# Kernel tuning notes

Hardware: AMD Instinct MI355X
Metric: run time of the kernel (lower is better)

Reference implementation:

```python
import jax, jax.numpy as jnp
import numpy as np

# hyperparameters from init_kwargs
STEPSZ = 0.1
ALPHA = 0.01
BETA = 0.01
NSTEPS = 50
DMAX = 15.0
EXTGRADFAC = 10.0
B, H, W, N = 2, 256, 256, 128


def _bilerp(field, pts):
    # field: [H, W]; pts: [N, 2] as (row, col) float coords -> [N]
    h, w = field.shape
    y = jnp.clip(pts[:, 0], 0.0, h - 1.001)
    x = jnp.clip(pts[:, 1], 0.0, w - 1.001)
    y0 = jnp.floor(y).astype(jnp.int32)
    x0 = jnp.floor(x).astype(jnp.int32)
    y1 = y0 + 1
    x1 = x0 + 1
    wy = y - y0.astype(field.dtype)
    wx = x - x0.astype(field.dtype)
    return (field[y0, x0] * (1 - wy) * (1 - wx)
            + field[y0, x1] * (1 - wy) * wx
            + field[y1, x0] * wy * (1 - wx)
            + field[y1, x1] * wy * wx)


def _evolve(pred, nodes):
    # pred: [H, W] distance-map prediction; nodes: [N, 2] closed-contour points
    gy = jnp.gradient(pred, axis=0)
    gx = jnp.gradient(pred, axis=1)
    hi = jnp.array([pred.shape[0] - 1.0, pred.shape[1] - 1.0], dtype=pred.dtype)

    def step(x, _):
        # internal forces: 2nd derivative (elasticity) and 4th derivative (rigidity)
        d2 = jnp.roll(x, -1, 0) + jnp.roll(x, 1, 0) - 2.0 * x
        d4 = jnp.roll(d2, -1, 0) + jnp.roll(d2, 1, 0) - 2.0 * d2
        # external force: descend the predicted distance map
        ext = -EXTGRADFAC * jnp.stack([_bilerp(gy, x), _bilerp(gx, x)], axis=-1)
        x = x + STEPSZ * (ALPHA * d2 - BETA * d4 + ext)
        x = jnp.clip(x, 0.0, hi)
        return x, None

    x, _ = jax.lax.scan(step, nodes, None, length=NSTEPS)
    return x


def _render(nodes):
    # distance from every pixel to the nearest snake segment, clamped at DMAX
    yy, xx = jnp.meshgrid(jnp.arange(H, dtype=nodes.dtype),
                          jnp.arange(W, dtype=nodes.dtype), indexing='ij')
    q = jnp.stack([yy, xx], axis=-1).reshape(-1, 2)          # [P, 2]
    p0 = nodes                                               # [N, 2]
    p1 = jnp.roll(nodes, -1, 0)                              # closed contour
    d = p1 - p0                                              # [N, 2]
    dd = jnp.sum(d * d, axis=-1) + 1e-8                      # [N]
    qp = q[:, None, :] - p0[None, :, :]                      # [P, N, 2]
    t = jnp.clip(jnp.sum(qp * d[None], axis=-1) / dd, 0.0, 1.0)  # [P, N]
    r = qp - t[..., None] * d[None]                          # residual to projection
    dist = jnp.sqrt(jnp.sum(r * r, axis=-1) + 1e-12)         # [P, N]
    return jnp.minimum(dist.min(axis=1), DMAX).reshape(H, W)


def setup_inputs() -> dict:
    key = jax.random.key(0)
    k1, k2 = jax.random.split(key)
    pred_dmap = jax.random.normal(k1, (B, 1, H, W), dtype=jnp.float32)
    # snake control points spread over the image
    nodes = jax.random.uniform(k2, (B, N, 2), dtype=jnp.float32) * (H - 1.0)
    return {"pred_dmap": pred_dmap, "nodes": nodes}


def reference(pred_dmap, nodes):
    pred = pred_dmap[:, 0]                                   # [B, H, W] (detached in torch)
    final_nodes = jax.vmap(_evolve)(jax.lax.stop_gradient(pred), nodes)
    snake_dm = jax.vmap(_render)(final_nodes)[:, None]       # [B, 1, H, W]
    snake_dm = jax.lax.stop_gradient(snake_dm)               # noGrad: snake path detached
    loss = jnp.mean(jnp.square(pred_dmap - snake_dm))
    return loss
```

## Files before the change

kernel.cpp:

```cpp
#include <hip/hip_runtime.h>

#define HH 256
#define WW 256
#define NB 2
#define NN 128
#define NSTEPS_K 50
#define NBLK 256
#define MAGIC_G 0x11C0FFEE
#define MAGIC_E 0x22C0FFEE
#define MAGIC_R 0x33C0FFEE
#define SPIN_G 200000
#define SPIN_E 60000
#define SPIN_R 60000

#define WS_PART   0
#define WS_GFLG   256
#define WS_RFLG   512
#define WS_EREP   1024
#define WS_FNODE  2048
#define WS_FIELD  4096
#define WS_NEEDED_BYTES ((WS_FIELD + (size_t)NB * HH * WW * 2) * 4)

static __device__ __forceinline__ int ld_i(int* p) {
    return __hip_atomic_load(p, __ATOMIC_RELAXED, __HIP_MEMORY_SCOPE_AGENT);
}
static __device__ __forceinline__ void st_i(int* p, int v) {
    __hip_atomic_store(p, v, __ATOMIC_RELAXED, __HIP_MEMORY_SCOPE_AGENT);
}
static __device__ __forceinline__ unsigned long long ld_u64(unsigned long long* p) {
    return __hip_atomic_load(p, __ATOMIC_RELAXED, __HIP_MEMORY_SCOPE_AGENT);
}
static __device__ __forceinline__ void st_u64(unsigned long long* p, unsigned long long v) {
    __hip_atomic_store(p, v, __ATOMIC_RELAXED, __HIP_MEMORY_SCOPE_AGENT);
}
static __device__ __forceinline__ float ld_f(float* p) {
    return __hip_atomic_load(p, __ATOMIC_RELAXED, __HIP_MEMORY_SCOPE_AGENT);
}
static __device__ __forceinline__ void st_f(float* p, float v) {
    __hip_atomic_store(p, v, __ATOMIC_RELAXED, __HIP_MEMORY_SCOPE_AGENT);
}
union F2U { float2 f2; unsigned long long u; };

__global__ __launch_bounds__(1024) void fused2_kernel(
        const float* __restrict__ pred,
        const float* __restrict__ nodes_in,
        float* __restrict__ ws,
        float* __restrict__ out) {
    float* partials = ws + WS_PART;
    int*   g_flags  = (int*)(ws + WS_GFLG);
    int*   r_flags  = (int*)(ws + WS_RFLG);
    int*   e_rep    = (int*)(ws + WS_EREP);
    unsigned long long* fnodes_u = (unsigned long long*)(ws + WS_FNODE);
    unsigned long long* field_u  = (unsigned long long*)(ws + WS_FIELD);
    const float2*       field_f2 = (const float2*)(ws + WS_FIELD);

    const int blk = blockIdx.x;
    const int tid = threadIdx.x;
    const int myBatch = blk >> 7;

    if (tid < 512) {
        int idx = blk * 512 + tid;
        int b = idx >> 16, p = idx & 0xFFFF;
        int i = p >> 8, j = p & (WW - 1);
        const float* f = pred + (b << 16);
        int iu = max(i - 1, 0), id = min(i + 1, HH - 1);
        int jl = max(j - 1, 0), jr = min(j + 1, WW - 1);
        float sy = (i == 0 || i == HH - 1) ? 1.0f : 0.5f;
        float sx = (j == 0 || j == WW - 1) ? 1.0f : 0.5f;
        F2U cv;
        cv.f2 = make_float2(sy * (f[(id << 8) + j] - f[(iu << 8) + j]),
                            sx * (f[(i << 8) + jr] - f[(i << 8) + jl]));
        st_u64(&field_u[idx], cv.u);
    }
    __syncthreads();
    if (tid == 0) st_i(&g_flags[blk], MAGIC_G);

    if (blk < NB) {
        const int b = blk;
        if (tid < 64) {
            int f0 = b * 128 + tid * 2;
            for (int it = 0; it < SPIN_G; ++it) {
                bool ok = (ld_i(&g_flags[f0]) == MAGIC_G) &&
                          (ld_i(&g_flags[f0 + 1]) == MAGIC_G);
                if (__all(ok)) break;
                __builtin_amdgcn_s_sleep(2);
            }
        }
        __syncthreads();

        const float2* gb = field_f2 + (b << 16);
        float acc = 0.0f;
        #pragma unroll
        for (int k = 0; k < 8; ++k) acc += gb[((k << 10) + tid) << 3].x;
        asm volatile("" :: "v"(acc));
        __syncthreads();

        if (tid < 64) {
            const int l = tid;
            const int pl = (l + 63) & 63;
            const int nl = (l + 1) & 63;
            float4 nd = ((const float4*)nodes_in)[b * 64 + l];
            float y0n = nd.x, x0n = nd.y;
            float y1n = nd.z, x1n = nd.w;

            __builtin_amdgcn_s_setprio(1);
            for (int s = 0; s < NSTEPS_K; ++s) {
                float yca = fminf(fmaxf(y0n, 0.0f), 254.999f);
                float xca = fminf(fmaxf(x0n, 0.0f), 254.999f);
                int ra = (int)yca, ca = (int)xca;
                float wya = yca - (float)ra, wxa = xca - (float)ca;
                int basea = (ra << 8) + ca;
                float2 a00 = gb[basea],       a01 = gb[basea + 1];
                float2 a10 = gb[basea + WW],  a11 = gb[basea + WW + 1];

                float ycb = fminf(fmaxf(y1n, 0.0f), 254.999f);
                float xcb = fminf(fmaxf(x1n, 0.0f), 254.999f);
                int rb = (int)ycb, cb = (int)xcb;
                float wyb = ycb - (float)rb, wxb = xcb - (float)cb;
                int baseb = (rb << 8) + cb;
                float2 b00 = gb[baseb],       b01 = gb[baseb + 1];
                float2 b10 = gb[baseb + WW],  b11 = gb[baseb + WW + 1];

                float pya = __shfl(y0n, pl), pxa = __shfl(x0n, pl);
                float pyb = __shfl(y1n, pl), pxb = __shfl(x1n, pl);
                float nya = __shfl(y0n, nl), nxa = __shfl(x0n, nl);
                float nyb = __shfl(y1n, nl), nxb = __shfl(x1n, nl);

                float d2ya = (y1n + pyb) - 2.0f * y0n;
                float d2xa = (x1n + pxb) - 2.0f * x0n;
                float d2yb = (nya + y0n) - 2.0f * y1n;
                float d2xb = (nxa + x0n) - 2.0f * x1n;
                float d2pyb = (y0n + pya) - 2.0f * pyb;
                float d2pxb = (x0n + pxa) - 2.0f * pxb;
                float d2nya = (nyb + y1n) - 2.0f * nya;
                float d2nxa = (nxb + x1n) - 2.0f * nxa;

                float d4ya = (d2yb + d2pyb) - 2.0f * d2ya;
                float d4xa = (d2xb + d2pxb) - 2.0f * d2xa;
                float d4yb = (d2nya + d2ya) - 2.0f * d2yb;
                float d4xb = (d2nxa + d2xa) - 2.0f * d2xb;

                float ua = 1.0f - wya, va = 1.0f - wxa;
                float bya = a00.x * ua * va + a01.x * ua * wxa + a10.x * wya * va + a11.x * wya * wxa;
                float bxa = a00.y * ua * va + a01.y * ua * wxa + a10.y * wya * va + a11.y * wya * wxa;
                float ub = 1.0f - wyb, vb = 1.0f - wxb;
                float byb = b00.x * ub * vb + b01.x * ub * wxb + b10.x * wyb * vb + b11.x * wyb * wxb;
                float bxb = b00.y * ub * vb + b01.y * ub * wxb + b10.y * wyb * vb + b11.y * wyb * wxb;

                y0n = y0n + 0.1f * ((0.01f * d2ya - 0.01f * d4ya) + (-10.0f * bya));
                x0n = x0n + 0.1f * ((0.01f * d2xa - 0.01f * d4xa) + (-10.0f * bxa));
                y1n = y1n + 0.1f * ((0.01f * d2yb - 0.01f * d4yb) + (-10.0f * byb));
                x1n = x1n + 0.1f * ((0.01f * d2xb - 0.01f * d4xb) + (-10.0f * bxb));
                y0n = fminf(fmaxf(y0n, 0.0f), 255.0f);
                x0n = fminf(fmaxf(x0n, 0.0f), 255.0f);
                y1n = fminf(fmaxf(y1n, 0.0f), 255.0f);
                x1n = fminf(fmaxf(x1n, 0.0f), 255.0f);
            }
            __builtin_amdgcn_s_setprio(0);

            F2U c0, c1;
            c0.f2 = make_float2(y0n, x0n);
            c1.f2 = make_float2(y1n, x1n);
            st_u64(&fnodes_u[b * 128 + 2 * l], c0.u);
            st_u64(&fnodes_u[b * 128 + 2 * l + 1], c1.u);
            asm volatile("s_waitcnt vmcnt(0)" ::: "memory");
            if (l == 0) {
                #pragma unroll
                for (int k = 0; k < 8; ++k) st_i(&e_rep[(b * 8 + k) * 64], MAGIC_E);
            }
        }
        __syncthreads();
    }

    if (tid == 0) {
        int* rep = &e_rep[(myBatch * 8 + (blk & 7)) * 64];
        for (int it = 0; it < SPIN_E; ++it) {
            if (ld_i(rep) == MAGIC_E) break;
            __builtin_amdgcn_s_sleep(32);
        }
    }
    __syncthreads();

    __shared__ float nny[NN], nnx[NN];
    __shared__ float p0y[NN], p0x[NN], sdy[NN], sdx[NN], sidd[NN];
    if (tid < NN) {
        F2U cv; cv.u = ld_u64(&fnodes_u[myBatch * 128 + tid]);
        nny[tid] = cv.f2.x; nnx[tid] = cv.f2.y;
    }
    __syncthreads();
    if (tid < NN) {
        float ay = nny[tid], ax = nnx[tid];
        int j = (tid + 1) & (NN - 1);
        float cy = nny[j], cx = nnx[j];
        float ddy = cy - ay, ddx = cx - ax;
        p0y[tid] = ay; p0x[tid] = ax;
        sdy[tid] = ddy; sdx[tid] = ddx;
        sidd[tid] = 1.0f / (ddy * ddy + ddx * ddx + 1e-8f);
    }
    __syncthreads();

    float se = 0.0f;
    if (tid < 512) {
        int pixin = (blk & 127) * 512 + tid;
        float qy = (float)(pixin >> 8);
        float qx = (float)(pixin & (WW - 1));
        float minr2 = 1e30f;
        #pragma unroll 8
        for (int s = 0; s < NN; ++s) {
            float qpy = qy - p0y[s];
            float qpx = qx - p0x[s];
            float t = (qpy * sdy[s] + qpx * sdx[s]) * sidd[s];
            t = fminf(fmaxf(t, 0.0f), 1.0f);
            float ry = qpy - t * sdy[s];
            float rx = qpx - t * sdx[s];
            minr2 = fminf(minr2, ry * ry + rx * rx);
        }
        float dist = fminf(sqrtf(minr2 + 1e-12f), 15.0f);
        float e = pred[(myBatch << 16) + pixin] - dist;
        se = e * e;
    }
    for (int off = 32; off > 0; off >>= 1) se += __shfl_down(se, off);
    __shared__ float red[16];
    if ((tid & 63) == 0) red[tid >> 6] = se;
    __syncthreads();
    if (tid == 0) {
        float p = 0.0f;
        #pragma unroll
        for (int w = 0; w < 8; ++w) p += red[w];
        st_f(&partials[blk], p);
        asm volatile("s_waitcnt vmcnt(0)" ::: "memory");
        st_i(&r_flags[blk], MAGIC_R);
    }

    if (blk == 0 && tid < 64) {
        for (int it = 0; it < SPIN_R; ++it) {
            bool ok = (ld_i(&r_flags[tid*4+0]) == MAGIC_R) &&
                      (ld_i(&r_flags[tid*4+1]) == MAGIC_R) &&
                      (ld_i(&r_flags[tid*4+2]) == MAGIC_R) &&
                      (ld_i(&r_flags[tid*4+3]) == MAGIC_R);
            if (__all(ok)) break;
            __builtin_amdgcn_s_sleep(8);
        }
        float s = 0.0f;
        #pragma unroll
        for (int k = 0; k < 4; ++k)
            s += ld_f(&partials[tid + (k << 6)]);
        for (int off = 32; off > 0; off >>= 1) s += __shfl_down(s, off);
        if (tid == 0) out[0] = s * (1.0f / (float)(NB * HH * WW));
        #pragma unroll
        for (int k = 0; k < 4; ++k) { st_i(&g_flags[tid*4+k], 0); st_i(&r_flags[tid*4+k], 0); }
        if (tid < 16) st_i(&e_rep[tid * 64], 0);
    }
}

__device__ __forceinline__ void sample_grad_direct(const float* __restrict__ f,
                                                   float y, float x,
                                                   float& by, float& bx) {
    float yc = fminf(fmaxf(y, 0.0f), 254.999f);
    float xc = fminf(fmaxf(x, 0.0f), 254.999f);
    int r0 = (int)yc, c0 = (int)xc;
    int r1 = r0 + 1, c1 = c0 + 1;
    float wy = yc - (float)r0, wx = xc - (float)c0;
    int rm = max(r0 - 1, 0), rp = min(r1 + 1, HH - 1);
    int cm = max(c0 - 1, 0), cp = min(c1 + 1, WW - 1);
    float sy0 = (r0 == 0) ? 1.0f : 0.5f;
    float sy1 = (r1 == HH - 1) ? 1.0f : 0.5f;
    float sx0 = (c0 == 0) ? 1.0f : 0.5f;
    float sx1 = (c1 == WW - 1) ? 1.0f : 0.5f;
    const float* fr0 = f + (r0 << 8);
    const float* fr1 = f + (r1 << 8);
    const float* frm = f + (rm << 8);
    const float* frp = f + (rp << 8);
    float f00 = fr0[c0], f01 = fr0[c1];
    float f10 = fr1[c0], f11 = fr1[c1];
    float f0m = fr0[cm], f0p = fr0[cp];
    float f1m = fr1[cm], f1p = fr1[cp];
    float fm0 = frm[c0], fm1 = frm[c1];
    float fp0 = frp[c0], fp1 = frp[c1];
    float gy00 = sy0 * (f10 - fm0), gy01 = sy0 * (f11 - fm1);
    float gy10 = sy1 * (fp0 - f00), gy11 = sy1 * (fp1 - f01);
    float gx00 = sx0 * (f01 - f0m), gx01 = sx1 * (f0p - f00);
    float gx10 = sx0 * (f11 - f1m), gx11 = sx1 * (f1p - f10);
    float u = 1.0f - wy, v = 1.0f - wx;
    by = gy00 * u * v + gy01 * u * wx + gy10 * wy * v + gy11 * wy * wx;
    bx = gx00 * u * v + gx01 * u * wx + gx10 * wy * v + gx11 * wy * wx;
}

__global__ __launch_bounds__(64, 1) void evolve_direct_kernel(
        const float* __restrict__ pred,
        const float* __restrict__ nodes_in,
        float* __restrict__ nodes_out,
        int* __restrict__ counter) {
    const int b = blockIdx.x;
    const int l = threadIdx.x;
    if (b == 0 && l == 0)
        __hip_atomic_store(counter, 0, __ATOMIC_RELAXED, __HIP_MEMORY_SCOPE_AGENT);
    const float* f = pred + b * HH * WW;
    const int pl = (l + 63) & 63;
    const int nl = (l + 1) & 63;
    float4 nd = ((const float4*)nodes_in)[b * 64 + l];
    float y0n = nd.x, x0n = nd.y, y1n = nd.z, x1n = nd.w;
    for (int s = 0; s < NSTEPS_K; ++s) {
        float by0, bx0, by1, bx1;
        sample_grad_direct(f, y0n, x0n, by0, bx0);
        sample_grad_direct(f, y1n, x1n, by1, bx1);
        float pya = __shfl(y0n, pl), pxa = __shfl(x0n, pl);
        float pyb = __shfl(y1n, pl), pxb = __shfl(x1n, pl);
        float nya = __shfl(y0n, nl), nxa = __shfl(x0n, nl);
        float nyb = __shfl(y1n, nl), nxb = __shfl(x1n, nl);
        float d2ya = (y1n + pyb) - 2.0f * y0n;
        float d2xa = (x1n + pxb) - 2.0f * x0n;
        float d2yb = (nya + y0n) - 2.0f * y1n;
        float d2xb = (nxa + x0n) - 2.0f * x1n;
        float d2pyb = (y0n + pya) - 2.0f * pyb;
        float d2pxb = (x0n + pxa) - 2.0f * pxb;
        float d2nya = (nyb + y1n) - 2.0f * nya;
        float d2nxa = (nxb + x1n) - 2.0f * nxa;
        float d4ya = (d2yb + d2pyb) - 2.0f * d2ya;
        float d4xa = (d2xb + d2pxb) - 2.0f * d2xa;
        float d4yb = (d2nya + d2ya) - 2.0f * d2yb;
        float d4xb = (d2nxa + d2xa) - 2.0f * d2xb;
        y0n = y0n + 0.1f * ((0.01f * d2ya - 0.01f * d4ya) + (-10.0f * by0));
        x0n = x0n + 0.1f * ((0.01f * d2xa - 0.01f * d4xa) + (-10.0f * bx0));
        y1n = y1n + 0.1f * ((0.01f * d2yb - 0.01f * d4yb) + (-10.0f * by1));
        x1n = x1n + 0.1f * ((0.01f * d2xb - 0.01f * d4xb) + (-10.0f * bx1));
        y0n = fminf(fmaxf(y0n, 0.0f), 255.0f);
        x0n = fminf(fmaxf(x0n, 0.0f), 255.0f);
        y1n = fminf(fmaxf(y1n, 0.0f), 255.0f);
        x1n = fminf(fmaxf(x1n, 0.0f), 255.0f);
    }
    float4 o4; o4.x = y0n; o4.y = x0n; o4.z = y1n; o4.w = x1n;
    ((float4*)nodes_out)[b * 64 + l] = o4;
}

#define RBLK ((HH * WW) / 256)
#define NPART (NB * RBLK)

__global__ void render_kernel(const float* __restrict__ pred,
                              const float* __restrict__ nodes,
                              float* __restrict__ partials,
                              int* __restrict__ counter,
                              float* __restrict__ out) {
    const int b = blockIdx.y;
    const int chunk = blockIdx.x;
    const int tid = threadIdx.x;
    __shared__ float p0y[NN], p0x[NN], sdy[NN], sdx[NN], sidd[NN];
    if (tid < NN) {
        float ay = nodes[(b * NN + tid) * 2 + 0];
        float ax = nodes[(b * NN + tid) * 2 + 1];
        int j = (tid + 1) & (NN - 1);
        float cy = nodes[(b * NN + j) * 2 + 0];
        float cx = nodes[(b * NN + j) * 2 + 1];
        float ddy = cy - ay, ddx = cx - ax;
        p0y[tid] = ay; p0x[tid] = ax;
        sdy[tid] = ddy; sdx[tid] = ddx;
        sidd[tid] = 1.0f / (ddy * ddy + ddx * ddx + 1e-8f);
    }
    __syncthreads();
    const int pix = chunk * 256 + tid;
    const float qy = (float)(pix >> 8);
    const float qx = (float)(pix & (WW - 1));
    float minr2 = 1e30f;
#pragma unroll 8
    for (int s = 0; s < NN; ++s) {
        float qpy = qy - p0y[s];
        float qpx = qx - p0x[s];
        float t = (qpy * sdy[s] + qpx * sdx[s]) * sidd[s];
        t = fminf(fmaxf(t, 0.0f), 1.0f);
        float ry = qpy - t * sdy[s];
        float rx = qpx - t * sdx[s];
        minr2 = fminf(minr2, ry * ry + rx * rx);
    }
    float dist = fminf(sqrtf(minr2 + 1e-12f), 15.0f);
    float e = pred[b * HH * WW + pix] - dist;
    float se = e * e;
    for (int off = 32; off > 0; off >>= 1) se += __shfl_down(se, off);
    __shared__ float red[4];
    if ((tid & 63) == 0) red[tid >> 6] = se;
    __syncthreads();
    __shared__ int lastBlk;
    if (tid == 0) {
        float p = (red[0] + red[1]) + (red[2] + red[3]);
        __hip_atomic_store(&partials[b * RBLK + chunk], p, __ATOMIC_RELEASE, __HIP_MEMORY_SCOPE_AGENT);
        int t = __hip_atomic_fetch_add(counter, 1, __ATOMIC_ACQ_REL, __HIP_MEMORY_SCOPE_AGENT);
        lastBlk = (t == NPART - 1);
    }
    __syncthreads();
    if (lastBlk) {
        float v = __hip_atomic_load(&partials[tid], __ATOMIC_RELAXED, __HIP_MEMORY_SCOPE_AGENT)
                + __hip_atomic_load(&partials[tid + 256], __ATOMIC_RELAXED, __HIP_MEMORY_SCOPE_AGENT);
        for (int off = 32; off > 0; off >>= 1) v += __shfl_down(v, off);
        __shared__ float red2[4];
        if ((tid & 63) == 0) red2[tid >> 6] = v;
        __syncthreads();
        if (tid == 0)
            out[0] = ((red2[0] + red2[1]) + (red2[2] + red2[3])) * (1.0f / (float)(NB * HH * WW));
    }
}

extern "C" void kernel_launch(void* const* d_in, const int* in_sizes, int n_in,
                              void* d_out, int out_size, void* d_ws, size_t ws_size,
                              hipStream_t stream) {
    const float* pred = (const float*)d_in[0];
    const float* nodes = (const float*)d_in[1];
    float* ws = (float*)d_ws;

    if (ws_size >= WS_NEEDED_BYTES) {
        fused2_kernel<<<dim3(NBLK), dim3(1024), 0, stream>>>(pred, nodes, ws, (float*)d_out);
    } else {
        float* partials = ws;
        float* fnodes = ws + 512;
        int* counter = (int*)(ws + 1024);
        evolve_direct_kernel<<<dim3(NB), dim3(64), 0, stream>>>(pred, nodes, fnodes, counter);
        render_kernel<<<dim3(RBLK, NB), dim3(256), 0, stream>>>(pred, fnodes, partials,
                                                                counter, (float*)d_out);
    }
}
```

Before: 48.37 us.

## Overlap per-wave gradient-flag waits with cache warming and merge bilinear loads

```diff
diff --git a/kernel.cpp b/kernel.cpp
--- a/kernel.cpp
+++ b/kernel.cpp
@@ -9,9 +9,9 @@
 #define MAGIC_G 0x11C0FFEE
 #define MAGIC_E 0x22C0FFEE
 #define MAGIC_R 0x33C0FFEE
-#define SPIN_G 200000
-#define SPIN_E 60000
-#define SPIN_R 60000
+#define SPIN_G 400000
+#define SPIN_E 120000
+#define SPIN_R 120000
 
 #define WS_PART   0
 #define WS_GFLG   256
@@ -41,7 +41,14 @@
 }
 union F2U { float2 f2; unsigned long long u; };
 
-__global__ __launch_bounds__(1024) void fused2_kernel(
+typedef float f4v __attribute__((ext_vector_type(4)));
+static __device__ __forceinline__ f4v ld_pair(const float2* p) {
+    f4v r;
+    __builtin_memcpy(&r, p, sizeof(f4v));
+    return r;
+}
+
+__global__ __launch_bounds__(1024) void fused3_kernel(
         const float* __restrict__ pred,
         const float* __restrict__ nodes_in,
         float* __restrict__ ws,
@@ -77,22 +84,22 @@
 
     if (blk < NB) {
         const int b = blk;
-        if (tid < 64) {
-            int f0 = b * 128 + tid * 2;
-            for (int it = 0; it < SPIN_G; ++it) {
-                bool ok = (ld_i(&g_flags[f0]) == MAGIC_G) &&
-                          (ld_i(&g_flags[f0 + 1]) == MAGIC_G);
-                if (__all(ok)) break;
-                __builtin_amdgcn_s_sleep(2);
+        const float2* gb = field_f2 + (b << 16);
+
+        {
+            const int w = tid >> 6, ln = tid & 63;
+            float acc = 0.0f;
+            #pragma unroll
+            for (int k = 0; k < 8; ++k) {
+                int* fl = &g_flags[b * 128 + k * 16 + w];
+                for (int it = 0; it < SPIN_G; ++it) {
+                    if (ld_i(fl) == MAGIC_G) break;
+                    __builtin_amdgcn_s_sleep(1);
+                }
+                acc += gb[(k * 1024 + w * 64 + ln) << 3].x;
             }
+            asm volatile("" :: "v"(acc));
         }
-        __syncthreads();
-
-        const float2* gb = field_f2 + (b << 16);
-        float acc = 0.0f;
-        #pragma unroll
-        for (int k = 0; k < 8; ++k) acc += gb[((k << 10) + tid) << 3].x;
-        asm volatile("" :: "v"(acc));
         __syncthreads();
 
         if (tid < 64) {
@@ -110,16 +117,16 @@
                 int ra = (int)yca, ca = (int)xca;
                 float wya = yca - (float)ra, wxa = xca - (float)ca;
                 int basea = (ra << 8) + ca;
-                float2 a00 = gb[basea],       a01 = gb[basea + 1];
-                float2 a10 = gb[basea + WW],  a11 = gb[basea + WW + 1];
+                f4v ra0 = ld_pair(&gb[basea]);
+                f4v ra1 = ld_pair(&gb[basea + WW]);
 
                 float ycb = fminf(fmaxf(y1n, 0.0f), 254.999f);
                 float xcb = fminf(fmaxf(x1n, 0.0f), 254.999f);
                 int rb = (int)ycb, cb = (int)xcb;
                 float wyb = ycb - (float)rb, wxb = xcb - (float)cb;
                 int baseb = (rb << 8) + cb;
-                float2 b00 = gb[baseb],       b01 = gb[baseb + 1];
-                float2 b10 = gb[baseb + WW],  b11 = gb[baseb + WW + 1];
+                f4v rb0 = ld_pair(&gb[baseb]);
+                f4v rb1 = ld_pair(&gb[baseb + WW]);
 
                 float pya = __shfl(y0n, pl), pxa = __shfl(x0n, pl);
                 float pyb = __shfl(y1n, pl), pxb = __shfl(x1n, pl);
@@ -141,11 +148,11 @@
                 float d4xb = (d2nxa + d2xa) - 2.0f * d2xb;
 
                 float ua = 1.0f - wya, va = 1.0f - wxa;
-                float bya = a00.x * ua * va + a01.x * ua * wxa + a10.x * wya * va + a11.x * wya * wxa;
-                float bxa = a00.y * ua * va + a01.y * ua * wxa + a10.y * wya * va + a11.y * wya * wxa;
+                float bya = ra0[0] * ua * va + ra0[2] * ua * wxa + ra1[0] * wya * va + ra1[2] * wya * wxa;
+                float bxa = ra0[1] * ua * va + ra0[3] * ua * wxa + ra1[1] * wya * va + ra1[3] * wya * wxa;
                 float ub = 1.0f - wyb, vb = 1.0f - wxb;
-                float byb = b00.x * ub * vb + b01.x * ub * wxb + b10.x * wyb * vb + b11.x * wyb * wxb;
-                float bxb = b00.y * ub * vb + b01.y * ub * wxb + b10.y * wyb * vb + b11.y * wyb * wxb;
+                float byb = rb0[0] * ub * vb + rb0[2] * ub * wxb + rb1[0] * wyb * vb + rb1[2] * wyb * wxb;
+                float bxb = rb0[1] * ub * vb + rb0[3] * ub * wxb + rb1[1] * wyb * vb + rb1[3] * wyb * wxb;
 
                 y0n = y0n + 0.1f * ((0.01f * d2ya - 0.01f * d4ya) + (-10.0f * bya));
                 x0n = x0n + 0.1f * ((0.01f * d2xa - 0.01f * d4xa) + (-10.0f * bxa));
@@ -176,7 +183,7 @@
         int* rep = &e_rep[(myBatch * 8 + (blk & 7)) * 64];
         for (int it = 0; it < SPIN_E; ++it) {
             if (ld_i(rep) == MAGIC_E) break;
-            __builtin_amdgcn_s_sleep(32);
+            __builtin_amdgcn_s_sleep(8);
         }
     }
     __syncthreads();
@@ -406,7 +413,7 @@
     float* ws = (float*)d_ws;
 
     if (ws_size >= WS_NEEDED_BYTES) {
-        fused2_kernel<<<dim3(NBLK), dim3(1024), 0, stream>>>(pred, nodes, ws, (float*)d_out);
+        fused3_kernel<<<dim3(NBLK), dim3(1024), 0, stream>>>(pred, nodes, ws, (float*)d_out);
     } else {
         float* partials = ws;
         float* fnodes = ws + 512;
```

New measurement: 47.09 us. -2.6%, faster.
